# Performance work log

Measured on AMD Instinct MI355X. Metric: run time of the kernel, lower is better.

The kernel has to match this reference:

```python
import jax, jax.numpy as jnp
import numpy as np

DIM = 1024
N_HEADS = 16
HEAD_DIM = DIM // N_HEADS  # 64
THETA = 10000.0
B, S = 4, 1024


def _rope_full_dim(x):
    """RoPE applied over the FULL last dim (head_dim == model dim), matching the
    original module which builds RotaryEmbeddings(head_dim=args.dim) and applies
    it to [B, S, dim] before splitting into heads. Positions start at 0."""
    Bx, Sx, D = x.shape
    freq = 1.0 / (THETA ** (jnp.arange(0, D, 2, dtype=jnp.float32) / D))  # [D/2]
    ang = jnp.arange(Sx, dtype=jnp.float32)[:, None] * freq[None, :]      # [S, D/2]
    cos, sin = jnp.cos(ang), jnp.sin(ang)
    xp = x.astype(jnp.float32).reshape(Bx, Sx, D // 2, 2)
    x0, x1 = xp[..., 0], xp[..., 1]
    rot = jnp.stack([x0 * cos - x1 * sin, x0 * sin + x1 * cos], axis=-1)
    return rot.reshape(Bx, Sx, D).astype(x.dtype)


def setup_inputs() -> dict:
    key = jax.random.key(0)
    ks = jax.random.split(key, 5)
    scale = 1.0 / np.sqrt(DIM)
    x = jax.random.normal(ks[0], (B, S, DIM), dtype=jnp.float32)
    Wq = jax.random.normal(ks[1], (DIM, DIM), dtype=jnp.float32) * scale
    Wk = jax.random.normal(ks[2], (DIM, DIM), dtype=jnp.float32) * scale
    Wv = jax.random.normal(ks[3], (DIM, DIM), dtype=jnp.float32) * scale
    Wo = jax.random.normal(ks[4], (DIM, DIM), dtype=jnp.float32) * scale
    bo = jnp.zeros((DIM,), dtype=jnp.float32)
    return {"x": x, "Wq": Wq, "Wk": Wk, "Wv": Wv, "Wo": Wo, "bo": bo, "start_pos": 0}


def reference(x, Wq, Wk, Wv, Wo, bo, start_pos):
    # start_pos == 0: the zero-initialized KV cache write+read is an identity
    # (keys == xk, values == xv over [:, :S]); n_rep == 1 so repeat_kv is a no-op.
    # NOTE: the original applies NO causal mask.
    Bx, Sx, _ = x.shape
    xq = _rope_full_dim(x @ Wq.T)  # [B, S, DIM] (weights stored torch-style [out,in])
    xk = _rope_full_dim(x @ Wk.T)
    xv = x @ Wv.T
    q = xq.reshape(Bx, Sx, N_HEADS, HEAD_DIM).transpose(0, 2, 1, 3)  # [B,H,S,D]
    k = xk.reshape(Bx, Sx, N_HEADS, HEAD_DIM).transpose(0, 2, 1, 3)
    v = xv.reshape(Bx, Sx, N_HEADS, HEAD_DIM).transpose(0, 2, 1, 3)
    scores = jnp.einsum("bhqd,bhkd->bhqk", q, k) / np.float32(np.sqrt(HEAD_DIM))
    attn = jax.nn.softmax(scores.astype(jnp.float32), axis=-1).astype(q.dtype)
    out = jnp.einsum("bhqk,bhkd->bhqd", attn, v)          # [B,H,S,D]
    out = out.transpose(0, 2, 1, 3).reshape(Bx, Sx, DIM)  # [B,S,DIM]
    return out @ Wo.T + bo
```

## Files before the change

### kernel.cpp

```cpp
#include <hip/hip_runtime.h>
#include <cstdint>
#include <cstddef>

typedef _Float16 f16;
typedef __attribute__((ext_vector_type(8))) _Float16 h8v;
typedef __attribute__((ext_vector_type(4))) _Float16 h4v;
typedef __attribute__((ext_vector_type(2))) _Float16 h2v;
typedef __attribute__((ext_vector_type(4))) float f4v;

#define DIM 1024
#define SEQ 1024
#define NH 16
#define HD 64

#if __has_builtin(__builtin_amdgcn_exp2f)
#define EXP2(x) __builtin_amdgcn_exp2f(x)
#else
#define EXP2(x) exp2f(x)
#endif
#if __has_builtin(__builtin_amdgcn_rcpf)
#define RCP(x) __builtin_amdgcn_rcpf(x)
#else
#define RCP(x) (1.0f / (x))
#endif

__device__ __forceinline__ void gld16(const void* g, void* l) {
  __builtin_amdgcn_global_load_lds(
      (const __attribute__((address_space(1))) void*)g,
      (__attribute__((address_space(3))) void*)l, 16, 0, 0);
}

__device__ __forceinline__ f4v mfma16(h8v a, h8v b, f4v c) {
  return __builtin_amdgcn_mfma_f32_16x16x32_f16(a, b, c, 0, 0, 0);
}
__device__ __forceinline__ f4v mfma16k16(h4v a, h4v b, f4v c) {
  return __builtin_amdgcn_mfma_f32_16x16x16f16(a, b, c, 0, 0, 0);
}

__device__ __forceinline__ h4v pk4(float a, float b, float c, float d) {
  h2v lo = __builtin_bit_cast(h2v, __builtin_amdgcn_cvt_pkrtz(a, b));
  h2v hi = __builtin_bit_cast(h2v, __builtin_amdgcn_cvt_pkrtz(c, d));
  return (h4v){lo[0], lo[1], hi[0], hi[1]};
}

__device__ __forceinline__ void cvt_store4(f16* dst, float4 v) {
  *(h4v*)dst = (h4v){(f16)v.x, (f16)v.y, (f16)v.z, (f16)v.w};
}

__global__ __launch_bounds__(256) void convert_kernel(
    const float* __restrict__ x,  const float* __restrict__ Wq,
    const float* __restrict__ Wk, const float* __restrict__ Wv,
    const float* __restrict__ Wo,
    f16* __restrict__ xh, f16* __restrict__ wqkv, f16* __restrict__ woh)
{
  int i = blockIdx.x * 256 + threadIdx.x;
  cvt_store4(xh + 4 * (size_t)i, ((const float4*)x)[i]);
  if (i < DIM * DIM / 4) {
    cvt_store4(wqkv + 4 * (size_t)i,               ((const float4*)Wq)[i]);
    cvt_store4(wqkv + DIM * DIM + 4 * (size_t)i,   ((const float4*)Wk)[i]);
    cvt_store4(wqkv + 2 * DIM * DIM + 4 * (size_t)i, ((const float4*)Wv)[i]);
    cvt_store4(woh + 4 * (size_t)i,                ((const float4*)Wo)[i]);
  }
}

__global__ __launch_bounds__(256) void qkv_gemm(
    const f16* __restrict__ A, const f16* __restrict__ W,
    f16* __restrict__ Qh, f16* __restrict__ Kh, f16* __restrict__ Vt)
{
  __shared__ f16 lA[128 * 32];
  __shared__ f16 lB[128 * 32];
  const int m0 = blockIdx.x * 128;
  const int n0 = blockIdx.y * 128;
  const int tid = threadIdx.x;
  const int w = tid >> 6, lane = tid & 63, quad = lane >> 4, l16 = lane & 15;
  const int wm = (w >> 1) * 64, wn = (w & 1) * 64;

  const int c0 = tid, c1 = 256 + tid;
  const int r0 = c0 >> 2, kc0 = (c0 & 3) ^ ((r0 >> 1) & 3);
  const int r1 = c1 >> 2, kc1 = (c1 & 3) ^ ((r1 >> 1) & 3);
  const f16* gA0 = A + (size_t)(m0 + r0) * DIM + kc0 * 8;
  const f16* gA1 = A + (size_t)(m0 + r1) * DIM + kc1 * 8;
  const f16* gB0 = W + (size_t)(n0 + r0) * DIM + kc0 * 8;
  const f16* gB1 = W + (size_t)(n0 + r1) * DIM + kc1 * 8;
  f16* lA0 = &lA[(c0 & ~63) * 8];
  f16* lA1 = &lA[(c1 & ~63) * 8];
  f16* lB0 = &lB[(c0 & ~63) * 8];
  f16* lB1 = &lB[(c1 & ~63) * 8];

  int pA[4], pB[4];
#pragma unroll
  for (int t = 0; t < 4; ++t) {
    int r = wm + t * 16 + l16;
    pA[t] = r * 4 + (quad ^ ((r >> 1) & 3));
    int rn = wn + t * 16 + l16;
    pB[t] = rn * 4 + (quad ^ ((rn >> 1) & 3));
  }

  f4v acc[4][4] = {};
  for (int kt = 0; kt < DIM / 32; ++kt) {
    const int ko = kt * 32;
    gld16(gA0 + ko, lA0);
    gld16(gA1 + ko, lA1);
    gld16(gB0 + ko, lB0);
    gld16(gB1 + ko, lB1);
    __syncthreads();
    h8v af[4], bf[4];
#pragma unroll
    for (int t = 0; t < 4; ++t) af[t] = *(const h8v*)&lA[pA[t] * 8];
#pragma unroll
    for (int t = 0; t < 4; ++t) bf[t] = *(const h8v*)&lB[pB[t] * 8];
#pragma unroll
    for (int i = 0; i < 4; ++i)
#pragma unroll
      for (int j = 0; j < 4; ++j)
        acc[i][j] = mfma16(af[i], bf[j], acc[i][j]);
    __syncthreads();
  }

  if (n0 < 2 * DIM) {
    f16* dst = (n0 < DIM) ? Qh : Kh;
    const float osc = (n0 < DIM) ? 0.18033688f : 1.0f;
    const float sgn = (l16 & 1) ? 1.0f : -1.0f;
#pragma unroll
    for (int j = 0; j < 4; ++j) {
      const int n = n0 + wn + j * 16 + l16;
      const int d = n & (DIM - 1);
      const float fr = exp2f(-0.025952563f * (float)(d >> 1));
      const float frr = fr * 0.15915494f;
      const int hh = d >> 6, dd = d & 63;
#pragma unroll
      for (int i = 0; i < 4; ++i) {
        const int mb = m0 + wm + i * 16 + quad * 4;
#pragma unroll
        for (int r = 0; r < 4; ++r) {
          const int m = mb + r;
          const int s = m & (SEQ - 1), b = m >> 10;
          const float v = acc[i][j][r];
          const float pt = __shfl_xor(v, 1, 64);
          float sn, cs;
#if __has_builtin(__builtin_amdgcn_sinf) && __has_builtin(__builtin_amdgcn_cosf)
          float ar = (float)s * frr;
          ar -= truncf(ar);
          sn = __builtin_amdgcn_sinf(ar);
          cs = __builtin_amdgcn_cosf(ar);
#else
          float ang = (float)s * fr;
          sn = __sinf(ang); cs = __cosf(ang);
#endif
          dst[((size_t)(b * NH + hh) * SEQ + s) * HD + dd] =
              (f16)((v * cs + sgn * pt * sn) * osc);
        }
      }
    }
  } else {
#pragma unroll
    for (int i = 0; i < 4; ++i) {
      const int mb = m0 + wm + i * 16 + quad * 4;
      const int b = mb >> 10;
      const int sp = ((mb & (SEQ - 1)) & ~63) + quad * 16 + i * 4;
#pragma unroll
      for (int j = 0; j < 4; ++j) {
        const int d = (n0 - 2 * DIM) + wn + j * 16 + l16;
        const int hh = d >> 6, dd = d & 63;
        h4v vv = {(f16)acc[i][j][0], (f16)acc[i][j][1],
                  (f16)acc[i][j][2], (f16)acc[i][j][3]};
        *(h4v*)&Vt[((size_t)(b * NH + hh) * HD + dd) * SEQ + sp] = vv;
      }
    }
  }
}

__global__ __launch_bounds__(256) void attn_kernel(
    const f16* __restrict__ Q, const f16* __restrict__ K,
    const f16* __restrict__ V, f16* __restrict__ O)
{
  __shared__ f16 LK[2][4096];
  __shared__ f16 LV[2][4096];
  const int tid = threadIdx.x;
  const int w = tid >> 6, lane = tid & 63, quad = lane >> 4, l16 = lane & 15;
  const int bid = blockIdx.x;
  const int qt = bid >> 6, bh = bid & 63;
  const f16* Qb = Q + (size_t)bh * SEQ * HD;
  const f16* Kg = K + (size_t)bh * SEQ * HD;
  const f16* Vg = V + (size_t)bh * HD * SEQ;
  const int q0 = qt * 128 + w * 16;

  const h8v bq0a = *(const h8v*)&Qb[(size_t)(q0 + l16) * HD + quad * 8];
  const h8v bq0b = *(const h8v*)&Qb[(size_t)(q0 + l16) * HD + quad * 8 + 32];
  const h8v bq1a = *(const h8v*)&Qb[(size_t)(q0 + 64 + l16) * HD + quad * 8];
  const h8v bq1b = *(const h8v*)&Qb[(size_t)(q0 + 64 + l16) * HD + quad * 8 + 32];

  const int c0 = tid, c1 = 256 + tid;
  const int r0 = c0 >> 3, kc0 = (c0 & 7) ^ (r0 & 7);
  const int r1 = c1 >> 3, kc1 = (c1 & 7) ^ (r1 & 7);
  const f16* gK0 = Kg + (size_t)r0 * HD + kc0 * 8;
  const f16* gK1 = Kg + (size_t)r1 * HD + kc1 * 8;
  const f16* gV0 = Vg + (size_t)r0 * SEQ + kc0 * 8;
  const f16* gV1 = Vg + (size_t)r1 * SEQ + kc1 * 8;
  const int dk0 = (c0 & ~63) * 8, dk1 = (c1 & ~63) * 8;

  int koff[4][2];
#pragma unroll
  for (int j = 0; j < 4; ++j) {
    int r = j * 16 + l16;
#pragma unroll
    for (int kk = 0; kk < 2; ++kk)
      koff[j][kk] = (r * 8 + ((quad + 4 * kk) ^ (r & 7))) * 8;
  }
  int voff2[2];
#pragma unroll
  for (int jp = 0; jp < 2; ++jp)
    voff2[jp] = l16 * 64 + ((quad * 2 + jp) ^ (l16 & 7)) * 8;

  const h4v vones = {(f16)1.f, (f16)1.f, (f16)1.f, (f16)1.f};
  f4v accL0 = {}, accL1 = {};
  f4v accO0[4] = {}, accO1[4] = {};

#define ATTN_PREF(TT, BUF)                       \
  {                                              \
    const size_t kb = (size_t)(TT) * 64;         \
    gld16(gK0 + kb * HD, &LK[BUF][dk0]);         \
    gld16(gK1 + kb * HD, &LK[BUF][dk1]);         \
    gld16(gV0 + kb, &LV[BUF][dk0]);              \
    gld16(gV1 + kb, &LV[BUF][dk1]);              \
  }

#define ATTN_TILE(BUF)                                                       \
  {                                                                          \
    h8v kf[4][2];                                                            \
    _Pragma("unroll")                                                        \
    for (int j = 0; j < 4; ++j) {                                            \
      kf[j][0] = *(const h8v*)&LK[BUF][koff[j][0]];                          \
      kf[j][1] = *(const h8v*)&LK[BUF][koff[j][1]];                          \
    }                                                                        \
    f4v sc0[4], sc1[4];                                                      \
    _Pragma("unroll")                                                        \
    for (int j = 0; j < 4; ++j) {                                            \
      f4v z0 = {-12.f, -12.f, -12.f, -12.f};          \
      z0 = mfma16(kf[j][0], bq0a, z0);                                       \
      z0 = mfma16(kf[j][1], bq0b, z0);                                       \
      sc0[j] = z0;                                                           \
      f4v z1 = {-12.f, -12.f, -12.f, -12.f};                                 \
      z1 = mfma16(kf[j][0], bq1a, z1);                                       \
      z1 = mfma16(kf[j][1], bq1b, z1);                                       \
      sc1[j] = z1;                                                           \
    }                                                                        \
    h4v pf0[4], pf1[4];                                                      \
    _Pragma("unroll")                                                        \
    for (int j = 0; j < 4; ++j) {                                            \
      pf0[j] = pk4(EXP2(sc0[j][0]), EXP2(sc0[j][1]),                         \
                   EXP2(sc0[j][2]), EXP2(sc0[j][3]));                        \
      pf1[j] = pk4(EXP2(sc1[j][0]), EXP2(sc1[j][1]),                         \
                   EXP2(sc1[j][2]), EXP2(sc1[j][3]));                        \
    }                                                                        \
    h4v ps0 = (pf0[0] + pf0[1]) + (pf0[2] + pf0[3]);                         \
    h4v ps1 = (pf1[0] + pf1[1]) + (pf1[2] + pf1[3]);                         \
    accL0 = mfma16k16(ps0, vones, accL0);                                    \
    accL1 = mfma16k16(ps1, vones, accL1);                                    \
    _Pragma("unroll")                                                        \
    for (int dt = 0; dt < 4; ++dt) {                                         \
      _Pragma("unroll")                                                      \
      for (int jp = 0; jp < 2; ++jp) {                                       \
        const h8v vv = *(const h8v*)&LV[BUF][voff2[jp] + dt * 1024];         \
        const h4v vlo = __builtin_shufflevector(vv, vv, 0, 1, 2, 3);         \
        const h4v vhi = __builtin_shufflevector(vv, vv, 4, 5, 6, 7);         \
        accO0[dt] = mfma16k16(pf0[2 * jp], vlo, accO0[dt]);                  \
        accO1[dt] = mfma16k16(pf1[2 * jp], vlo, accO1[dt]);                  \
        accO0[dt] = mfma16k16(pf0[2 * jp + 1], vhi, accO0[dt]);              \
        accO1[dt] = mfma16k16(pf1[2 * jp + 1], vhi, accO1[dt]);              \
      }                                                                      \
    }                                                                        \
  }

  ATTN_PREF(0, 0);
  for (int t = 0; t < SEQ / 64; t += 2) {
    __syncthreads();
    ATTN_PREF(t + 1, 1);
    ATTN_TILE(0);
    __syncthreads();
    if (t + 2 < SEQ / 64) ATTN_PREF(t + 2, 0);
    ATTN_TILE(1);
  }
#undef ATTN_PREF
#undef ATTN_TILE

  f4v inv0, inv1;
#pragma unroll
  for (int r = 0; r < 4; ++r) { inv0[r] = RCP(accL0[r]); inv1[r] = RCP(accL1[r]); }

  const int b = bh >> 4, hh = bh & 15;
#pragma unroll
  for (int dt = 0; dt < 4; ++dt) {
    const int d = dt * 16 + l16;
#pragma unroll
    for (int r = 0; r < 4; ++r) {
      const int s0 = q0 + quad * 4 + r;
      O[(size_t)(b * SEQ + s0) * DIM + hh * HD + d] =
          (f16)(accO0[dt][r] * inv0[r]);
      O[(size_t)(b * SEQ + s0 + 64) * DIM + hh * HD + d] =
          (f16)(accO1[dt][r] * inv1[r]);
    }
  }
}

__global__ __launch_bounds__(256) void out_gemm(
    const f16* __restrict__ A, const f16* __restrict__ W,
    const float* __restrict__ bias, float* __restrict__ out)
{
  __shared__ f16 lA[64 * 32];
  __shared__ f16 lB[128 * 32];
  const int m0 = blockIdx.x * 64;
  const int n0 = blockIdx.y * 128;
  const int tid = threadIdx.x;
  const int w = tid >> 6, lane = tid & 63, quad = lane >> 4, l16 = lane & 15;
  const int wm = (w >> 1) * 32, wn = (w & 1) * 64;

  const int c0 = tid, c1 = 256 + tid;
  const int rA = c0 >> 2, kcA = (c0 & 3) ^ ((rA >> 1) & 3);
  const int rB1 = c1 >> 2, kcB1 = (c1 & 3) ^ ((rB1 >> 1) & 3);
  const f16* gA  = A + (size_t)(m0 + rA) * DIM + kcA * 8;
  const f16* gB0 = W + (size_t)(n0 + rA) * DIM + kcA * 8;
  const f16* gB1 = W + (size_t)(n0 + rB1) * DIM + kcB1 * 8;
  f16* lAp  = &lA[(c0 & ~63) * 8];
  f16* lB0p = &lB[(c0 & ~63) * 8];
  f16* lB1p = &lB[(c1 & ~63) * 8];

  int pA_[2], pB_[4];
#pragma unroll
  for (int t = 0; t < 2; ++t) {
    int r = wm + t * 16 + l16;
    pA_[t] = r * 4 + (quad ^ ((r >> 1) & 3));
  }
#pragma unroll
  for (int t = 0; t < 4; ++t) {
    int rn = wn + t * 16 + l16;
    pB_[t] = rn * 4 + (quad ^ ((rn >> 1) & 3));
  }

  f4v acc[2][4] = {};
  for (int kt = 0; kt < DIM / 32; ++kt) {
    const int ko = kt * 32;
    gld16(gA + ko, lAp);
    gld16(gB0 + ko, lB0p);
    gld16(gB1 + ko, lB1p);
    __syncthreads();
    h8v af[2], bf[4];
#pragma unroll
    for (int t = 0; t < 2; ++t) af[t] = *(const h8v*)&lA[pA_[t] * 8];
#pragma unroll
    for (int t = 0; t < 4; ++t) bf[t] = *(const h8v*)&lB[pB_[t] * 8];
#pragma unroll
    for (int i = 0; i < 2; ++i)
#pragma unroll
      for (int j = 0; j < 4; ++j)
        acc[i][j] = mfma16(af[i], bf[j], acc[i][j]);
    __syncthreads();
  }

#pragma unroll
  for (int i = 0; i < 2; ++i) {
#pragma unroll
    for (int j = 0; j < 4; ++j) {
      const int n = n0 + wn + j * 16 + l16;
      const float bv = bias[n];
#pragma unroll
      for (int r = 0; r < 4; ++r) {
        const int m = m0 + wm + i * 16 + quad * 4 + r;
        out[(size_t)m * DIM + n] = acc[i][j][r] + bv;
      }
    }
  }
}

extern "C" void kernel_launch(void* const* d_in, const int* in_sizes, int n_in,
                              void* d_out, int out_size, void* d_ws, size_t ws_size,
                              hipStream_t stream)
{
  (void)in_sizes; (void)n_in; (void)out_size; (void)ws_size;
  const float* x  = (const float*)d_in[0];
  const float* Wq = (const float*)d_in[1];
  const float* Wk = (const float*)d_in[2];
  const float* Wv = (const float*)d_in[3];
  const float* Wo = (const float*)d_in[4];
  const float* bo = (const float*)d_in[5];
  float* out = (float*)d_out;

  char* ws = (char*)d_ws;
  const size_t MB = (size_t)1 << 20;
  f16* xh   = (f16*)(ws);
  f16* wqkv = (f16*)(ws + 8  * MB);
  f16* woh  = (f16*)(ws + 14 * MB);
  f16* Qh   = (f16*)(ws + 16 * MB);
  f16* Kh   = (f16*)(ws + 24 * MB);
  f16* Vt   = (f16*)(ws + 32 * MB);
  f16* Oh   = (f16*)(ws);

  convert_kernel<<<dim3(4096), 256, 0, stream>>>(x, Wq, Wk, Wv, Wo, xh, wqkv, woh);
  qkv_gemm<<<dim3(32, 24), 256, 0, stream>>>(xh, wqkv, Qh, Kh, Vt);
  attn_kernel<<<dim3(512), 256, 0, stream>>>(Qh, Kh, Vt, Oh);
  out_gemm<<<dim3(64, 8), 256, 0, stream>>>(Oh, woh, bo, out);
}
```

Measured before the change: 173.6 us.

## Double-buffer LDS tiles in both GEMMs and rebalance the conversion kernel

The QKV and output GEMMs now use two LDS buffers per operand. The loads for the next K-tile are issued before the MFMAs on the current tile, so global-to-LDS transfers overlap compute, and one of the two barriers per tile is gone. The conversion kernel now gives every thread four equal float4 conversions across x and the four weights, replacing the old scheme where only the first quarter of threads also converted weights. This doubles LDS use per block, which may lower occupancy.

```diff
diff --git a/kernel.cpp b/kernel.cpp
--- a/kernel.cpp
+++ b/kernel.cpp
@@ -53,13 +53,31 @@
     const float* __restrict__ Wo,
     f16* __restrict__ xh, f16* __restrict__ wqkv, f16* __restrict__ woh)
 {
+  const int NX = DIM * SEQ;
+  const int NW = DIM * DIM / 4;
   int i = blockIdx.x * 256 + threadIdx.x;
-  cvt_store4(xh + 4 * (size_t)i, ((const float4*)x)[i]);
-  if (i < DIM * DIM / 4) {
-    cvt_store4(wqkv + 4 * (size_t)i,               ((const float4*)Wq)[i]);
-    cvt_store4(wqkv + DIM * DIM + 4 * (size_t)i,   ((const float4*)Wk)[i]);
-    cvt_store4(wqkv + 2 * DIM * DIM + 4 * (size_t)i, ((const float4*)Wv)[i]);
-    cvt_store4(woh + 4 * (size_t)i,                ((const float4*)Wo)[i]);
+#pragma unroll
+  for (int k = 0; k < 4; ++k, i += 524288) {
+    const float4* s;
+    f16* d;
+    if (i < NX) {
+      s = (const float4*)x + i;            d = xh + 4 * (size_t)i;
+    } else {
+      int j = i - NX;
+      if (j < NW) {
+        s = (const float4*)Wq + j;         d = wqkv + 4 * (size_t)j;
+      } else if (j < 2 * NW) {
+        j -= NW;
+        s = (const float4*)Wk + j;         d = wqkv + DIM * DIM + 4 * (size_t)j;
+      } else if (j < 3 * NW) {
+        j -= 2 * NW;
+        s = (const float4*)Wv + j;         d = wqkv + 2 * DIM * DIM + 4 * (size_t)j;
+      } else {
+        j -= 3 * NW;
+        s = (const float4*)Wo + j;         d = woh + 4 * (size_t)j;
+      }
+    }
+    cvt_store4(d, *s);
   }
 }
 
@@ -67,8 +85,8 @@
     const f16* __restrict__ A, const f16* __restrict__ W,
     f16* __restrict__ Qh, f16* __restrict__ Kh, f16* __restrict__ Vt)
 {
-  __shared__ f16 lA[128 * 32];
-  __shared__ f16 lB[128 * 32];
+  __shared__ f16 lA[2][4096];
+  __shared__ f16 lB[2][4096];
   const int m0 = blockIdx.x * 128;
   const int n0 = blockIdx.y * 128;
   const int tid = threadIdx.x;
@@ -82,10 +100,7 @@
   const f16* gA1 = A + (size_t)(m0 + r1) * DIM + kc1 * 8;
   const f16* gB0 = W + (size_t)(n0 + r0) * DIM + kc0 * 8;
   const f16* gB1 = W + (size_t)(n0 + r1) * DIM + kc1 * 8;
-  f16* lA0 = &lA[(c0 & ~63) * 8];
-  f16* lA1 = &lA[(c1 & ~63) * 8];
-  f16* lB0 = &lB[(c0 & ~63) * 8];
-  f16* lB1 = &lB[(c1 & ~63) * 8];
+  const int d0 = (c0 & ~63) * 8, d1 = (c1 & ~63) * 8;
 
   int pA[4], pB[4];
 #pragma unroll
@@ -97,25 +112,41 @@
   }
 
   f4v acc[4][4] = {};
-  for (int kt = 0; kt < DIM / 32; ++kt) {
-    const int ko = kt * 32;
-    gld16(gA0 + ko, lA0);
-    gld16(gA1 + ko, lA1);
-    gld16(gB0 + ko, lB0);
-    gld16(gB1 + ko, lB1);
-    __syncthreads();
-    h8v af[4], bf[4];
-#pragma unroll
-    for (int t = 0; t < 4; ++t) af[t] = *(const h8v*)&lA[pA[t] * 8];
-#pragma unroll
-    for (int t = 0; t < 4; ++t) bf[t] = *(const h8v*)&lB[pB[t] * 8];
-#pragma unroll
-    for (int i = 0; i < 4; ++i)
-#pragma unroll
-      for (int j = 0; j < 4; ++j)
-        acc[i][j] = mfma16(af[i], bf[j], acc[i][j]);
-    __syncthreads();
-  }
+
+#define QKV_PREF(KT, BUF)                  \
+  {                                        \
+    const int ko = (KT) * 32;              \
+    gld16(gA0 + ko, &lA[BUF][d0]);         \
+    gld16(gA1 + ko, &lA[BUF][d1]);         \
+    gld16(gB0 + ko, &lB[BUF][d0]);         \
+    gld16(gB1 + ko, &lB[BUF][d1]);         \
+  }
+
+#define QKV_COMP(BUF)                                                \
+  {                                                                  \
+    h8v af[4], bf[4];                                                \
+    _Pragma("unroll")                                                \
+    for (int t = 0; t < 4; ++t) af[t] = *(const h8v*)&lA[BUF][pA[t] * 8]; \
+    _Pragma("unroll")                                                \
+    for (int t = 0; t < 4; ++t) bf[t] = *(const h8v*)&lB[BUF][pB[t] * 8]; \
+    _Pragma("unroll")                                                \
+    for (int i = 0; i < 4; ++i)                                      \
+      _Pragma("unroll")                                              \
+      for (int j = 0; j < 4; ++j)                                    \
+        acc[i][j] = mfma16(af[i], bf[j], acc[i][j]);                 \
+  }
+
+  QKV_PREF(0, 0);
+  for (int kt = 0; kt < DIM / 32; kt += 2) {
+    __syncthreads();
+    QKV_PREF(kt + 1, 1);
+    QKV_COMP(0);
+    __syncthreads();
+    if (kt + 2 < DIM / 32) QKV_PREF(kt + 2, 0);
+    QKV_COMP(1);
+  }
+#undef QKV_PREF
+#undef QKV_COMP
 
   if (n0 < 2 * DIM) {
     f16* dst = (n0 < DIM) ? Qh : Kh;
@@ -307,8 +338,8 @@
     const f16* __restrict__ A, const f16* __restrict__ W,
     const float* __restrict__ bias, float* __restrict__ out)
 {
-  __shared__ f16 lA[64 * 32];
-  __shared__ f16 lB[128 * 32];
+  __shared__ f16 lA[2][2048];
+  __shared__ f16 lB[2][4096];
   const int m0 = blockIdx.x * 64;
   const int n0 = blockIdx.y * 128;
   const int tid = threadIdx.x;
@@ -321,9 +352,7 @@
   const f16* gA  = A + (size_t)(m0 + rA) * DIM + kcA * 8;
   const f16* gB0 = W + (size_t)(n0 + rA) * DIM + kcA * 8;
   const f16* gB1 = W + (size_t)(n0 + rB1) * DIM + kcB1 * 8;
-  f16* lAp  = &lA[(c0 & ~63) * 8];
-  f16* lB0p = &lB[(c0 & ~63) * 8];
-  f16* lB1p = &lB[(c1 & ~63) * 8];
+  const int dA = (c0 & ~63) * 8, dB1 = (c1 & ~63) * 8;
 
   int pA_[2], pB_[4];
 #pragma unroll
@@ -338,24 +367,40 @@
   }
 
   f4v acc[2][4] = {};
-  for (int kt = 0; kt < DIM / 32; ++kt) {
-    const int ko = kt * 32;
-    gld16(gA + ko, lAp);
-    gld16(gB0 + ko, lB0p);
-    gld16(gB1 + ko, lB1p);
-    __syncthreads();
-    h8v af[2], bf[4];
-#pragma unroll
-    for (int t = 0; t < 2; ++t) af[t] = *(const h8v*)&lA[pA_[t] * 8];
-#pragma unroll
-    for (int t = 0; t < 4; ++t) bf[t] = *(const h8v*)&lB[pB_[t] * 8];
-#pragma unroll
-    for (int i = 0; i < 2; ++i)
-#pragma unroll
-      for (int j = 0; j < 4; ++j)
-        acc[i][j] = mfma16(af[i], bf[j], acc[i][j]);
-    __syncthreads();
-  }
+
+#define OUT_PREF(KT, BUF)                  \
+  {                                        \
+    const int ko = (KT) * 32;              \
+    gld16(gA + ko, &lA[BUF][dA]);          \
+    gld16(gB0 + ko, &lB[BUF][dA]);         \
+    gld16(gB1 + ko, &lB[BUF][dB1]);        \
+  }
+
+#define OUT_COMP(BUF)                                                 \
+  {                                                                   \
+    h8v af[2], bf[4];                                                 \
+    _Pragma("unroll")                                                 \
+    for (int t = 0; t < 2; ++t) af[t] = *(const h8v*)&lA[BUF][pA_[t] * 8]; \
+    _Pragma("unroll")                                                 \
+    for (int t = 0; t < 4; ++t) bf[t] = *(const h8v*)&lB[BUF][pB_[t] * 8]; \
+    _Pragma("unroll")                                                 \
+    for (int i = 0; i < 2; ++i)                                       \
+      _Pragma("unroll")                                               \
+      for (int j = 0; j < 4; ++j)                                     \
+        acc[i][j] = mfma16(af[i], bf[j], acc[i][j]);                  \
+  }
+
+  OUT_PREF(0, 0);
+  for (int kt = 0; kt < DIM / 32; kt += 2) {
+    __syncthreads();
+    OUT_PREF(kt + 1, 1);
+    OUT_COMP(0);
+    __syncthreads();
+    if (kt + 2 < DIM / 32) OUT_PREF(kt + 2, 0);
+    OUT_COMP(1);
+  }
+#undef OUT_PREF
+#undef OUT_COMP
 
 #pragma unroll
   for (int i = 0; i < 2; ++i) {
@@ -395,7 +440,7 @@
   f16* Vt   = (f16*)(ws + 32 * MB);
   f16* Oh   = (f16*)(ws);
 
-  convert_kernel<<<dim3(4096), 256, 0, stream>>>(x, Wq, Wk, Wv, Wo, xh, wqkv, woh);
+  convert_kernel<<<dim3(2048), 256, 0, stream>>>(x, Wq, Wk, Wv, Wo, xh, wqkv, woh);
   qkv_gemm<<<dim3(32, 24), 256, 0, stream>>>(xh, wqkv, Qh, Kh, Vt);
   attn_kernel<<<dim3(512), 256, 0, stream>>>(Qh, Kh, Vt, Oh);
   out_gemm<<<dim3(64, 8), 256, 0, stream>>>(Oh, woh, bo, out);
```

New measurement: 182.8 us. 1.05x slower.
